# Optimization experiments

Hardware: AMD Instinct MI355X
Metric: run time of the kernel (lower is better)

The kernel has to match this reference:

```python
import jax, jax.numpy as jnp
import numpy as np
import math

B, S, HID = 2, 2048, 2048
NH, NKV, HD, RD = 16, 4, 128, 64  # heads, kv heads, head_dim, rotary dim
G = NH // NKV                      # GQA group size = 4
EPS = 1e-6
THETA = 10000.0


def setup_inputs() -> dict:
    key = jax.random.key(0)
    k0, k1, k2 = jax.random.split(key, 3)
    hidden_states = jax.random.normal(k0, (B, S, HID), dtype=jnp.float32)
    # real rotary embeddings for rope_dim=64
    inv_freq = 1.0 / (THETA ** (jnp.arange(0, RD, 2, dtype=jnp.float32) / RD))  # [32]
    freqs = jnp.arange(S, dtype=jnp.float32)[:, None] * inv_freq[None, :]       # [S,32]
    emb = jnp.concatenate([freqs, freqs], axis=-1)                              # [S,64]
    cos = jnp.broadcast_to(jnp.cos(emb)[None], (B, S, RD)).astype(jnp.float32)
    sin = jnp.broadcast_to(jnp.sin(emb)[None], (B, S, RD)).astype(jnp.float32)
    w_qkv = jax.random.normal(k1, ((NH + 2 * NKV) * HD, HID), dtype=jnp.float32) * 0.02
    q_ln_w = jnp.ones((HD,), dtype=jnp.float32)
    k_ln_w = jnp.ones((HD,), dtype=jnp.float32)
    w_dense = jax.random.normal(k2, (HID, NH * HD), dtype=jnp.float32) * 0.02
    return {"hidden_states": hidden_states, "cos": cos, "sin": sin,
            "w_qkv": w_qkv, "q_ln_w": q_ln_w, "k_ln_w": k_ln_w, "w_dense": w_dense}


def _rmsnorm(x, w):
    xf = x.astype(jnp.float32)
    var = jnp.mean(xf * xf, axis=-1, keepdims=True)
    return (w * (xf * jax.lax.rsqrt(var + EPS)).astype(x.dtype))


def _rotate_half(x):
    x1, x2 = x[..., : x.shape[-1] // 2], x[..., x.shape[-1] // 2:]
    return jnp.concatenate([-x2, x1], axis=-1)


def reference(hidden_states, cos, sin, w_qkv, q_ln_w, k_ln_w, w_dense):
    bsz, q_len, _ = hidden_states.shape
    # fused QKV projection
    qkv = jnp.einsum('bsh,oh->bso', hidden_states, w_qkv)
    qkv = qkv.reshape(bsz, q_len, NH + 2 * NKV, HD)
    q = qkv[:, :, :NH].transpose(0, 2, 1, 3)            # [B,NH,S,HD]
    k = qkv[:, :, NH:NH + NKV].transpose(0, 2, 1, 3)    # [B,NKV,S,HD]
    v = qkv[:, :, NH + NKV:].transpose(0, 2, 1, 3)      # [B,NKV,S,HD]
    # per-head RMSNorm on Q/K
    q = _rmsnorm(q, q_ln_w)
    k = _rmsnorm(k, k_ln_w)
    # partial RoPE on first RD dims
    c = cos[:, None, :, :]  # [B,1,S,RD]
    s = sin[:, None, :, :]
    q_rot = q[..., :RD] * c + _rotate_half(q[..., :RD]) * s
    k_rot = k[..., :RD] * c + _rotate_half(k[..., :RD]) * s
    q = jnp.concatenate([q_rot, q[..., RD:]], axis=-1)
    k = jnp.concatenate([k_rot, k[..., RD:]], axis=-1)
    # GQA: group Q heads over KV heads (equivalent to repeat_kv)
    qg = q.reshape(bsz, NKV, G, q_len, HD)
    scale = 1.0 / math.sqrt(HD)
    scores = jnp.einsum('bgrqd,bgkd->bgrqk', qg, k) * scale   # [B,NKV,G,S,S]
    probs = jax.nn.softmax(scores.astype(jnp.float32), axis=-1).astype(q.dtype)
    out = jnp.einsum('bgrqk,bgkd->bgrqd', probs, v)           # [B,NKV,G,S,HD]
    out = out.reshape(bsz, NH, q_len, HD).transpose(0, 2, 1, 3).reshape(bsz, q_len, NH * HD)
    return jnp.einsum('bsd,od->bso', out, w_dense)
```

## Files before the change

### kernel.cpp

```cpp
#include <hip/hip_runtime.h>
#include <cstdint>
#include <cstddef>

typedef unsigned short u16;
typedef __attribute__((ext_vector_type(8))) short bf16x8;
typedef __attribute__((ext_vector_type(8))) u16   u16x8;
typedef __attribute__((ext_vector_type(4))) short short4v;
typedef __attribute__((ext_vector_type(4))) float f32x4;
typedef __attribute__((ext_vector_type(16))) float f32x16;
typedef __attribute__((ext_vector_type(4))) unsigned int u32x4;

#define DEVI static __device__ __forceinline__

constexpr int B_   = 2;
constexpr int S_   = 2048;
constexpr int HID_ = 2048;
constexpr int NH_  = 16;
constexpr int NKV_ = 4;
constexpr int HD_  = 128;
constexpr int TOK  = B_ * S_;
constexpr int OQKV = (NH_ + 2*NKV_) * HD_;

DEVI u16 f2bf(float f) {
  uint32_t u = __builtin_bit_cast(uint32_t, f);
  return (u16)((u + 0x7fffu + ((u >> 16) & 1u)) >> 16);
}
DEVI float bf2f(u16 h) { return __builtin_bit_cast(float, (uint32_t)h << 16); }

DEVI void gll16(const void* g, void* l) {
  __builtin_amdgcn_global_load_lds(
      (const __attribute__((address_space(1))) uint32_t*)g,
      (__attribute__((address_space(3))) uint32_t*)l, 16, 0, 0);
}

__global__ __launch_bounds__(256) void cvt3_kernel(
    const float* __restrict__ i0, u16* __restrict__ o0, int n0,
    const float* __restrict__ i1, u16* __restrict__ o1, int n1,
    const float* __restrict__ i2, u16* __restrict__ o2, int n2) {
  int idx = blockIdx.x * 256 + threadIdx.x;
  int stride = gridDim.x * 256;
#pragma unroll 1
  for (int pass = 0; pass < 3; ++pass) {
    const float* in = pass == 0 ? i0 : pass == 1 ? i1 : i2;
    u16* out       = pass == 0 ? o0 : pass == 1 ? o1 : o2;
    int n8         = pass == 0 ? n0 : pass == 1 ? n1 : n2;
    for (int i = idx; i < n8; i += stride) {
      const float4* p = reinterpret_cast<const float4*>(in) + (size_t)i * 2;
      float4 a = p[0], b = p[1];
      u16x8 v;
      v[0] = f2bf(a.x); v[1] = f2bf(a.y); v[2] = f2bf(a.z); v[3] = f2bf(a.w);
      v[4] = f2bf(b.x); v[5] = f2bf(b.y); v[6] = f2bf(b.z); v[7] = f2bf(b.w);
      reinterpret_cast<u16x8*>(out)[i] = v;
    }
  }
}

template <bool OUT_BF16>
__global__ __launch_bounds__(256) void gemm_bt_kernel(
    const u16* __restrict__ A, const u16* __restrict__ B, void* __restrict__ Cv,
    int M, int N, int K) {
  constexpr int BM = 128, BN = 128, BK = 32;
  __shared__ __align__(16) u16 As[2][BM * BK];
  __shared__ __align__(16) u16 Bs[2][BN * BK];
  const int tid  = threadIdx.x;
  const int lane = tid & 63;
  const int wid  = tid >> 6;
  const int bm = blockIdx.x * BM;
  const int bn = blockIdx.y * BN;
  const int wm = (wid >> 1) * 64;
  const int wn = (wid & 1) * 64;
  const int fr = lane & 15, fg = lane >> 4;

  const f32x4 fzero = {0.f, 0.f, 0.f, 0.f};
  f32x4 acc[4][4];
#pragma unroll
  for (int m = 0; m < 4; m++)
#pragma unroll
    for (int n = 0; n < 4; n++) acc[m][n] = fzero;

  auto stage = [&](int buf, int k0) {
#pragma unroll
    for (int i = 0; i < 2; i++) {
      int e = i * 256 + tid;
      gll16(A + (size_t)(bm + (e >> 2)) * K + (k0 + (e & 3) * 8), &As[buf][e * 8]);
    }
#pragma unroll
    for (int i = 0; i < 2; i++) {
      int e = i * 256 + tid;
      gll16(B + (size_t)(bn + (e >> 2)) * K + (k0 + (e & 3) * 8), &Bs[buf][e * 8]);
    }
  };

  stage(0, 0);
  __syncthreads();
  const int nt = K / BK;
  for (int t = 0; t < nt; ++t) {
    int cur = t & 1;
    if (t + 1 < nt) stage(cur ^ 1, (t + 1) * BK);
    bf16x8 af[4], bfv[4];
#pragma unroll
    for (int m = 0; m < 4; m++)
      af[m] = *reinterpret_cast<const bf16x8*>(&As[cur][(wm + m * 16 + fr) * BK + fg * 8]);
#pragma unroll
    for (int n = 0; n < 4; n++)
      bfv[n] = *reinterpret_cast<const bf16x8*>(&Bs[cur][(wn + n * 16 + fr) * BK + fg * 8]);
#pragma unroll
    for (int m = 0; m < 4; m++)
#pragma unroll
      for (int n = 0; n < 4; n++)
        acc[m][n] = __builtin_amdgcn_mfma_f32_16x16x32_bf16(af[m], bfv[n], acc[m][n], 0, 0, 0);
    __syncthreads();
  }

#pragma unroll
  for (int m = 0; m < 4; m++)
#pragma unroll
    for (int n = 0; n < 4; n++)
#pragma unroll
      for (int j = 0; j < 4; j++) {
        size_t row = bm + wm + m * 16 + fg * 4 + j;
        size_t col = bn + wn + n * 16 + fr;
        if constexpr (OUT_BF16)
          reinterpret_cast<u16*>(Cv)[row * N + col] = f2bf(acc[m][n][j]);
        else
          reinterpret_cast<float*>(Cv)[row * N + col] = acc[m][n][j];
      }
}

__global__ __launch_bounds__(256) void rmsrope_kernel(
    const u16* __restrict__ qkv, const float* __restrict__ cosb,
    const float* __restrict__ sinb, const float* __restrict__ qw,
    const float* __restrict__ kw, u16* __restrict__ Q, u16* __restrict__ K) {
  int gw   = blockIdx.x * 4 + (threadIdx.x >> 6);
  int lane = threadIdx.x & 63;
  int tok  = gw / 20;
  int slot = gw - tok * 20;
  if (tok >= TOK) return;
  int b = tok >> 11, s = tok & (S_ - 1);
  const u16* src = qkv + (size_t)tok * OQKV + slot * HD_;
  float x0 = bf2f(src[lane]);
  float x1 = bf2f(src[lane + 64]);
  float ss = x0 * x0 + x1 * x1;
#pragma unroll
  for (int m = 1; m < 64; m <<= 1) ss += __shfl_xor(ss, m, 64);
  float r = rsqrtf(ss * (1.0f / 128.0f) + 1e-6f);
  const float* w = (slot < 16) ? qw : kw;
  x0 *= r * w[lane];
  x1 *= r * w[lane + 64];
  float c  = cosb[(size_t)tok * 64 + lane];
  float sn = sinb[(size_t)tok * 64 + lane];
  float partner = __shfl_xor(x0, 32, 64);
  float rot = (lane < 32) ? -partner : partner;
  x0 = x0 * c + rot * sn;
  const float QSC = 0.12751743f;
  u16* dst;
  if (slot < 16) {
    x0 *= QSC; x1 *= QSC;
    dst = Q + (((size_t)b * NH_ + slot) * S_ + s) * HD_;
  } else {
    dst = K + (((size_t)b * NKV_ + (slot - 16)) * S_ + s) * HD_;
  }
  dst[lane]      = f2bf(x0);
  dst[lane + 64] = f2bf(x1);
}

__global__ __launch_bounds__(512, 2) void attn_kernel(
    const u16* __restrict__ Q, const u16* __restrict__ K,
    const u16* __restrict__ QKVb, u16* __restrict__ O) {
  __shared__ __align__(16) u16 Ks[2][64 * 128];
  __shared__ __align__(16) u16 Vt[2][128 * 64];
  __shared__ float rs_lds[8][32];
  const int tid  = threadIdx.x;
  const int lane = tid & 63, wid = tid >> 6;
  const int q32 = lane & 31, hi = lane >> 5;
  const int i_   = blockIdx.x;
  const int xcd  = i_ & 7, s_ = i_ >> 3;
  const int b = xcd >> 2, kvh = xcd & 3;
  const int h = kvh * 4 + (s_ & 3);
  const int qt = s_ >> 2;

  const u16* Qrow  = Q + ((size_t)(b * NH_ + h) * S_ + qt * 256 + wid * 32 + q32) * HD_;
  const u16* Kbase = K + (size_t)(b * NKV_ + kvh) * S_ * HD_;
  const u16* Vbase = QKVb + (size_t)b * S_ * OQKV + (size_t)(NH_ + NKV_) * HD_ + (size_t)kvh * HD_;

  bf16x8 qf[8];
#pragma unroll
  for (int m = 0; m < 8; m++)
    qf[m] = *reinterpret_cast<const bf16x8*>(Qrow + m * 16 + hi * 8);

  f32x16 acc[4];
#pragma unroll
  for (int n = 0; n < 4; n++)
#pragma unroll
    for (int r = 0; r < 16; r++) acc[n][r] = 0.f;

  float rs = 0.f;

  auto stageK = [&](int buf, int kt) {
#pragma unroll
    for (int i = 0; i < 2; i++) {
      int e = i * 512 + tid;
      int krow = e >> 4, ci = e & 15;
      int cs = ci ^ (krow & 15);
      gll16(Kbase + ((size_t)kt * 64 + krow) * HD_ + cs * 8, &Ks[buf][e * 8]);
    }
  };
  u16x8 vreg[4];
  auto loadV = [&](int kt) {
    if (tid < 256) {
      int kvb = tid >> 4, db = tid & 15;
#pragma unroll
      for (int i = 0; i < 4; i++)
        vreg[i] = *reinterpret_cast<const u16x8*>(
            Vbase + ((size_t)kt * 64 + kvb * 4 + i) * OQKV + db * 8);
    }
  };
  auto writeV = [&](int buf) {
    if (tid < 256) {
      int kvb = tid >> 4, db = tid & 15;
#pragma unroll
      for (int j = 0; j < 8; j++) {
        int d = db * 8 + j;
        int sw = (d ^ (d >> 3)) & 7;
        int off = d * 128 + ((((kvb >> 1) ^ sw)) << 4) + ((kvb & 1) << 3);
        short4v wv = {(short)vreg[0][j], (short)vreg[1][j],
                      (short)vreg[2][j], (short)vreg[3][j]};
        *reinterpret_cast<short4v*>(reinterpret_cast<char*>(Vt[buf]) + off) = wv;
      }
    }
  };

  stageK(0, 0);
  loadV(0);
  writeV(0);
  __syncthreads();

  const int NT = S_ / 64;
  for (int kt = 0; kt < NT; ++kt) {
    const int cur = kt & 1;
    if (kt + 1 < NT) { stageK(cur ^ 1, kt + 1); loadV(kt + 1); }

    const u16* kbp = &Ks[cur][(size_t)q32 * 128];
    const int swz = lane & 15;
    unsigned int pa[4][4];
#pragma unroll
    for (int kb = 0; kb < 2; kb++) {
      f32x16 s;
#pragma unroll
      for (int r = 0; r < 16; r++) s[r] = 0.f;
      __builtin_amdgcn_s_setprio(1);
#pragma unroll
      for (int m = 0; m < 8; m++) {
        bf16x8 kf = *reinterpret_cast<const bf16x8*>(
            kbp + kb * 32 * 128 + ((((m * 2 + hi) ^ swz)) << 3));
        s = __builtin_amdgcn_mfma_f32_32x32x16_bf16(kf, qf[m], s, 0, 0, 0);
      }
      __builtin_amdgcn_s_setprio(0);
      float p[16];
#pragma unroll
      for (int r = 0; r < 16; r++) {
        p[r] = exp2f(s[r]);
        rs += p[r];
      }
      unsigned int w[8];
#pragma unroll
      for (int m2 = 0; m2 < 8; m2++) {
        unsigned int wv;
        asm("v_cvt_pk_bf16_f32 %0, %1, %2" : "=v"(wv) : "v"(p[2 * m2]), "v"(p[2 * m2 + 1]));
        w[m2] = wv;
      }
#pragma unroll
      for (int tp = 0; tp < 2; tp++) {
        unsigned int a0 = w[4 * tp + 0], b0 = w[4 * tp + 2];
        unsigned int a1 = w[4 * tp + 1], b1 = w[4 * tp + 3];
        asm("v_permlane32_swap_b32 %0, %1" : "+v"(a0), "+v"(b0));
        asm("v_permlane32_swap_b32 %0, %1" : "+v"(a1), "+v"(b1));
        pa[kb * 2 + tp][0] = a0;
        pa[kb * 2 + tp][1] = a1;
        pa[kb * 2 + tp][2] = b0;
        pa[kb * 2 + tp][3] = b1;
      }
    }

#pragma unroll
    for (int t = 0; t < 4; t++) {
      union { u32x4 u; bf16x8 h; } pf;
      pf.u = (u32x4){pa[t][0], pa[t][1], pa[t][2], pa[t][3]};
      __builtin_amdgcn_s_setprio(1);
#pragma unroll
      for (int n = 0; n < 4; n++) {
        int d = n * 32 + q32;
        int sw = (d ^ (d >> 3)) & 7;
        bf16x8 vf = *reinterpret_cast<const bf16x8*>(
            reinterpret_cast<const char*>(Vt[cur]) + d * 128 + (((t * 2 + hi) ^ sw) << 4));
        acc[n] = __builtin_amdgcn_mfma_f32_32x32x16_bf16(pf.h, vf, acc[n], 0, 0, 0);
      }
      __builtin_amdgcn_s_setprio(0);
    }

    if (kt + 1 < NT) writeV(cur ^ 1);
    __syncthreads();
  }

  float rtot = rs + __shfl_xor(rs, 32, 64);
  if (lane < 32) rs_lds[wid][q32] = rtot;
  __syncthreads();
  float rinv[16];
#pragma unroll
  for (int r = 0; r < 16; r++)
    rinv[r] = 1.0f / rs_lds[wid][(r & 3) + 8 * (r >> 2) + 4 * hi];

  const int qrow0 = qt * 256 + wid * 32;
  u16* ob = O + ((size_t)b * S_ + qrow0) * HID_ + h * HD_ + q32;
#pragma unroll
  for (int n = 0; n < 4; n++)
#pragma unroll
    for (int r = 0; r < 16; r++) {
      int qr = (r & 3) + 8 * (r >> 2) + 4 * hi;
      ob[(size_t)qr * HID_ + n * 32] = f2bf(acc[n][r] * rinv[r]);
    }
}

extern "C" void kernel_launch(void* const* d_in, const int* in_sizes, int n_in,
                              void* d_out, int out_size, void* d_ws, size_t ws_size,
                              hipStream_t stream) {
  (void)in_sizes; (void)n_in; (void)out_size; (void)ws_size;
  const float* hs   = (const float*)d_in[0];
  const float* cosb = (const float*)d_in[1];
  const float* sinb = (const float*)d_in[2];
  const float* wqkv = (const float*)d_in[3];
  const float* qw   = (const float*)d_in[4];
  const float* kw   = (const float*)d_in[5];
  const float* wd   = (const float*)d_in[6];
  float* out = (float*)d_out;
  char* ws = (char*)d_ws;
  constexpr size_t MB = 1048576;
  u16* Xb    = (u16*)(ws + 0 * MB);
  u16* Wqkvb = (u16*)(ws + 16 * MB);
  u16* Wdb   = (u16*)(ws + 28 * MB);
  u16* QKVb  = (u16*)(ws + 36 * MB);
  u16* Qb    = (u16*)(ws + 60 * MB);
  u16* Kb    = (u16*)(ws + 76 * MB);
  u16* Ob    = (u16*)(ws + 80 * MB);

  cvt3_kernel<<<2048, 256, 0, stream>>>(hs, Xb, TOK * HID_ / 8,
                                        wqkv, Wqkvb, OQKV * HID_ / 8,
                                        wd, Wdb, HID_ * HID_ / 8);

  gemm_bt_kernel<true><<<dim3(TOK / 128, OQKV / 128), 256, 0, stream>>>(
      Xb, Wqkvb, QKVb, TOK, OQKV, HID_);

  rmsrope_kernel<<<TOK * 20 / 4, 256, 0, stream>>>(QKVb, cosb, sinb, qw, kw, Qb, Kb);

  attn_kernel<<<256, 512, 0, stream>>>(Qb, Kb, QKVb, Ob);

  gemm_bt_kernel<false><<<dim3(TOK / 128, HID_ / 128), 256, 0, stream>>>(
      Ob, Wdb, out, TOK, HID_, HID_);
}
```

Before: 224.0 us.

## Rewrite GEMM with 256x128x64 tiles, triple-buffered LDS, swizzle and 32x32 MFMA

```diff
diff --git a/kernel.cpp b/kernel.cpp
--- a/kernel.cpp
+++ b/kernel.cpp
@@ -56,74 +56,96 @@
 }
 
 template <bool OUT_BF16>
-__global__ __launch_bounds__(256) void gemm_bt_kernel(
+__global__ __launch_bounds__(512, 1) void gemm_bt2_kernel(
     const u16* __restrict__ A, const u16* __restrict__ B, void* __restrict__ Cv,
     int M, int N, int K) {
-  constexpr int BM = 128, BN = 128, BK = 32;
-  __shared__ __align__(16) u16 As[2][BM * BK];
-  __shared__ __align__(16) u16 Bs[2][BN * BK];
+  constexpr int BM = 256, BN = 128, BK = 64;
+  __shared__ __align__(16) u16 As[3][BM * BK];
+  __shared__ __align__(16) u16 Bs[3][BN * BK];
   const int tid  = threadIdx.x;
-  const int lane = tid & 63;
-  const int wid  = tid >> 6;
+  const int lane = tid & 63, wid = tid >> 6;
+  const int hi   = lane >> 5;
   const int bm = blockIdx.x * BM;
   const int bn = blockIdx.y * BN;
   const int wm = (wid >> 1) * 64;
   const int wn = (wid & 1) * 64;
-  const int fr = lane & 15, fg = lane >> 4;
-
-  const f32x4 fzero = {0.f, 0.f, 0.f, 0.f};
-  f32x4 acc[4][4];
-#pragma unroll
-  for (int m = 0; m < 4; m++)
-#pragma unroll
-    for (int n = 0; n < 4; n++) acc[m][n] = fzero;
-
-  auto stage = [&](int buf, int k0) {
+
+  f32x16 acc[2][2];
+#pragma unroll
+  for (int mf = 0; mf < 2; mf++)
+#pragma unroll
+    for (int nf = 0; nf < 2; nf++)
+#pragma unroll
+      for (int r = 0; r < 16; r++) acc[mf][nf][r] = 0.f;
+
+  auto stage = [&](int t) {
+    int buf = t % 3;
+    const int k0 = t * BK;
+#pragma unroll
+    for (int i = 0; i < 4; i++) {
+      int e = i * 512 + tid;
+      int row = e >> 3, c = e & 7;
+      int cs = c ^ (row & 7);
+      gll16(A + (size_t)(bm + row) * K + (k0 + cs * 8), &As[buf][e * 8]);
+    }
 #pragma unroll
     for (int i = 0; i < 2; i++) {
-      int e = i * 256 + tid;
-      gll16(A + (size_t)(bm + (e >> 2)) * K + (k0 + (e & 3) * 8), &As[buf][e * 8]);
-    }
-#pragma unroll
-    for (int i = 0; i < 2; i++) {
-      int e = i * 256 + tid;
-      gll16(B + (size_t)(bn + (e >> 2)) * K + (k0 + (e & 3) * 8), &Bs[buf][e * 8]);
+      int e = i * 512 + tid;
+      int row = e >> 3, c = e & 7;
+      int cs = c ^ (row & 7);
+      gll16(B + (size_t)(bn + row) * K + (k0 + cs * 8), &Bs[buf][e * 8]);
     }
   };
 
-  stage(0, 0);
-  __syncthreads();
   const int nt = K / BK;
+  stage(0);
+  stage(1);
+  asm volatile("s_waitcnt vmcnt(6)" ::: "memory");
+  __builtin_amdgcn_s_barrier();
+
+  const int r7 = lane & 7;
   for (int t = 0; t < nt; ++t) {
-    int cur = t & 1;
-    if (t + 1 < nt) stage(cur ^ 1, (t + 1) * BK);
-    bf16x8 af[4], bfv[4];
-#pragma unroll
-    for (int m = 0; m < 4; m++)
-      af[m] = *reinterpret_cast<const bf16x8*>(&As[cur][(wm + m * 16 + fr) * BK + fg * 8]);
-#pragma unroll
-    for (int n = 0; n < 4; n++)
-      bfv[n] = *reinterpret_cast<const bf16x8*>(&Bs[cur][(wn + n * 16 + fr) * BK + fg * 8]);
-#pragma unroll
-    for (int m = 0; m < 4; m++)
-#pragma unroll
-      for (int n = 0; n < 4; n++)
-        acc[m][n] = __builtin_amdgcn_mfma_f32_16x16x32_bf16(af[m], bfv[n], acc[m][n], 0, 0, 0);
-    __syncthreads();
+    const int cur = t % 3;
+    if (t + 2 < nt) stage(t + 2);
+    const u16* ab = &As[cur][(size_t)(wm + (lane & 31)) * BK];
+    const u16* bb = &Bs[cur][(size_t)(wn + (lane & 31)) * BK];
+#pragma unroll
+    for (int k16 = 0; k16 < 4; k16++) {
+      const int kc = k16 * 2 + hi;
+      bf16x8 af[2], bfr[2];
+#pragma unroll
+      for (int mf = 0; mf < 2; mf++)
+        af[mf] = *reinterpret_cast<const bf16x8*>(ab + mf * 32 * BK + ((kc ^ r7) << 3));
+#pragma unroll
+      for (int nf = 0; nf < 2; nf++)
+        bfr[nf] = *reinterpret_cast<const bf16x8*>(bb + nf * 32 * BK + ((kc ^ r7) << 3));
+      __builtin_amdgcn_s_setprio(1);
+#pragma unroll
+      for (int mf = 0; mf < 2; mf++)
+#pragma unroll
+        for (int nf = 0; nf < 2; nf++)
+          acc[mf][nf] = __builtin_amdgcn_mfma_f32_32x32x16_bf16(af[mf], bfr[nf], acc[mf][nf], 0, 0, 0);
+      __builtin_amdgcn_s_setprio(0);
+    }
+    if (t + 2 < nt)
+      asm volatile("s_waitcnt vmcnt(6)" ::: "memory");
+    else if (t + 1 < nt)
+      asm volatile("s_waitcnt vmcnt(0)" ::: "memory");
+    __builtin_amdgcn_s_barrier();
   }
 
 #pragma unroll
-  for (int m = 0; m < 4; m++)
-#pragma unroll
-    for (int n = 0; n < 4; n++)
-#pragma unroll
-      for (int j = 0; j < 4; j++) {
-        size_t row = bm + wm + m * 16 + fg * 4 + j;
-        size_t col = bn + wn + n * 16 + fr;
+  for (int mf = 0; mf < 2; mf++)
+#pragma unroll
+    for (int nf = 0; nf < 2; nf++)
+#pragma unroll
+      for (int r = 0; r < 16; r++) {
+        size_t row = bm + wm + mf * 32 + (r & 3) + 8 * (r >> 2) + 4 * hi;
+        size_t col = bn + wn + nf * 32 + (lane & 31);
         if constexpr (OUT_BF16)
-          reinterpret_cast<u16*>(Cv)[row * N + col] = f2bf(acc[m][n][j]);
+          reinterpret_cast<u16*>(Cv)[row * N + col] = f2bf(acc[mf][nf][r]);
         else
-          reinterpret_cast<float*>(Cv)[row * N + col] = acc[m][n][j];
+          reinterpret_cast<float*>(Cv)[row * N + col] = acc[mf][nf][r];
       }
 }
 
@@ -347,13 +369,13 @@
                                         wqkv, Wqkvb, OQKV * HID_ / 8,
                                         wd, Wdb, HID_ * HID_ / 8);
 
-  gemm_bt_kernel<true><<<dim3(TOK / 128, OQKV / 128), 256, 0, stream>>>(
+  gemm_bt2_kernel<true><<<dim3(TOK / 256, OQKV / 128), 512, 0, stream>>>(
       Xb, Wqkvb, QKVb, TOK, OQKV, HID_);
 
   rmsrope_kernel<<<TOK * 20 / 4, 256, 0, stream>>>(QKVb, cosb, sinb, qw, kw, Qb, Kb);
 
   attn_kernel<<<256, 512, 0, stream>>>(Qb, Kb, QKVb, Ob);
 
-  gemm_bt_kernel<false><<<dim3(TOK / 128, HID_ / 128), 256, 0, stream>>>(
+  gemm_bt2_kernel<false><<<dim3(TOK / 256, HID_ / 128), 512, 0, stream>>>(
       Ob, Wdb, out, TOK, HID_, HID_);
 }
```

Measured after the change: 254.9 us. 1.14x slower.

## Fuse per-head RMSNorm and RoPE into the QKV GEMM epilogue

Applied to the files above, without the earlier changes.

```diff
diff --git a/kernel.cpp b/kernel.cpp
--- a/kernel.cpp
+++ b/kernel.cpp
@@ -127,41 +127,138 @@
       }
 }
 
-__global__ __launch_bounds__(256) void rmsrope_kernel(
-    const u16* __restrict__ qkv, const float* __restrict__ cosb,
-    const float* __restrict__ sinb, const float* __restrict__ qw,
-    const float* __restrict__ kw, u16* __restrict__ Q, u16* __restrict__ K) {
-  int gw   = blockIdx.x * 4 + (threadIdx.x >> 6);
-  int lane = threadIdx.x & 63;
-  int tok  = gw / 20;
-  int slot = gw - tok * 20;
-  if (tok >= TOK) return;
-  int b = tok >> 11, s = tok & (S_ - 1);
-  const u16* src = qkv + (size_t)tok * OQKV + slot * HD_;
-  float x0 = bf2f(src[lane]);
-  float x1 = bf2f(src[lane + 64]);
-  float ss = x0 * x0 + x1 * x1;
-#pragma unroll
-  for (int m = 1; m < 64; m <<= 1) ss += __shfl_xor(ss, m, 64);
-  float r = rsqrtf(ss * (1.0f / 128.0f) + 1e-6f);
-  const float* w = (slot < 16) ? qw : kw;
-  x0 *= r * w[lane];
-  x1 *= r * w[lane + 64];
-  float c  = cosb[(size_t)tok * 64 + lane];
-  float sn = sinb[(size_t)tok * 64 + lane];
-  float partner = __shfl_xor(x0, 32, 64);
-  float rot = (lane < 32) ? -partner : partner;
-  x0 = x0 * c + rot * sn;
-  const float QSC = 0.12751743f;
-  u16* dst;
-  if (slot < 16) {
-    x0 *= QSC; x1 *= QSC;
-    dst = Q + (((size_t)b * NH_ + slot) * S_ + s) * HD_;
-  } else {
-    dst = K + (((size_t)b * NKV_ + (slot - 16)) * S_ + s) * HD_;
-  }
-  dst[lane]      = f2bf(x0);
-  dst[lane + 64] = f2bf(x1);
+__global__ __launch_bounds__(256) void gemm_qkv_kernel(
+    const u16* __restrict__ A, const u16* __restrict__ B,
+    u16* __restrict__ QKVb, u16* __restrict__ Qo, u16* __restrict__ Ko,
+    const float* __restrict__ cosb, const float* __restrict__ sinb,
+    const float* __restrict__ qw, const float* __restrict__ kw) {
+  constexpr int N = OQKV, K = HID_;
+  constexpr int BM = 128, BN = 128, BK = 32;
+  __shared__ __align__(16) u16 As[2][BM * BK];
+  __shared__ __align__(16) u16 Bs[2][BN * BK];
+  __shared__ float rsum[4][64];
+  const int tid  = threadIdx.x;
+  const int lane = tid & 63;
+  const int wid  = tid >> 6;
+  const int bm = blockIdx.x * BM;
+  const int bn = blockIdx.y * BN;
+  const int wm = (wid >> 1) * 64;
+  const int wn = (wid & 1) * 64;
+  const int fr = lane & 15, fg = lane >> 4;
+
+  const f32x4 fzero = {0.f, 0.f, 0.f, 0.f};
+  f32x4 acc[4][4];
+#pragma unroll
+  for (int m = 0; m < 4; m++)
+#pragma unroll
+    for (int n = 0; n < 4; n++) acc[m][n] = fzero;
+
+  auto stage = [&](int buf, int k0) {
+#pragma unroll
+    for (int i = 0; i < 2; i++) {
+      int e = i * 256 + tid;
+      gll16(A + (size_t)(bm + (e >> 2)) * K + (k0 + (e & 3) * 8), &As[buf][e * 8]);
+    }
+#pragma unroll
+    for (int i = 0; i < 2; i++) {
+      int e = i * 256 + tid;
+      gll16(B + (size_t)(bn + (e >> 2)) * K + (k0 + (e & 3) * 8), &Bs[buf][e * 8]);
+    }
+  };
+
+  stage(0, 0);
+  __syncthreads();
+  const int nt = K / BK;
+  for (int t = 0; t < nt; ++t) {
+    int cur = t & 1;
+    if (t + 1 < nt) stage(cur ^ 1, (t + 1) * BK);
+    bf16x8 af[4], bfv[4];
+#pragma unroll
+    for (int m = 0; m < 4; m++)
+      af[m] = *reinterpret_cast<const bf16x8*>(&As[cur][(wm + m * 16 + fr) * BK + fg * 8]);
+#pragma unroll
+    for (int n = 0; n < 4; n++)
+      bfv[n] = *reinterpret_cast<const bf16x8*>(&Bs[cur][(wn + n * 16 + fr) * BK + fg * 8]);
+#pragma unroll
+    for (int m = 0; m < 4; m++)
+#pragma unroll
+      for (int n = 0; n < 4; n++)
+        acc[m][n] = __builtin_amdgcn_mfma_f32_16x16x32_bf16(af[m], bfv[n], acc[m][n], 0, 0, 0);
+    __syncthreads();
+  }
+
+  const int slot = blockIdx.y;
+  if (slot >= 20) {
+#pragma unroll
+    for (int m = 0; m < 4; m++)
+#pragma unroll
+      for (int n = 0; n < 4; n++)
+#pragma unroll
+        for (int j = 0; j < 4; j++) {
+          size_t row = bm + wm + m * 16 + fg * 4 + j;
+          size_t col = bn + wn + n * 16 + fr;
+          QKVb[row * N + col] = f2bf(acc[m][n][j]);
+        }
+    return;
+  }
+
+  float ssq[16];
+#pragma unroll
+  for (int m = 0; m < 4; m++)
+#pragma unroll
+    for (int j = 0; j < 4; j++) {
+      float s2 = 0.f;
+#pragma unroll
+      for (int n = 0; n < 4; n++) { float v = acc[m][n][j]; s2 = fmaf(v, v, s2); }
+      ssq[m * 4 + j] = s2;
+    }
+#pragma unroll
+  for (int msk = 1; msk < 16; msk <<= 1)
+#pragma unroll
+    for (int i = 0; i < 16; i++) ssq[i] += __shfl_xor(ssq[i], msk, 64);
+  if (fr == 0) {
+#pragma unroll
+    for (int i = 0; i < 16; i++)
+      rsum[wid][(i >> 2) * 16 + fg * 4 + (i & 3)] = ssq[i];
+  }
+  __syncthreads();
+
+  const float* gam = (slot < 16) ? qw : kw;
+  const float g0 = gam[wn + fr],      g1 = gam[wn + 16 + fr];
+  const float g2 = gam[wn + 32 + fr], g3 = gam[wn + 48 + fr];
+  const float qsc = (slot < 16) ? 0.12751743f : 1.0f;
+
+#pragma unroll
+  for (int m = 0; m < 4; m++)
+#pragma unroll
+    for (int j = 0; j < 4; j++) {
+      const int i = m * 4 + j;
+      float tot = ssq[i] + rsum[wid ^ 1][m * 16 + fg * 4 + j];
+      float rv  = rsqrtf(tot * (1.0f / 128.0f) + 1e-6f);
+      size_t tok = (size_t)(bm + wm + m * 16 + fg * 4 + j);
+      float v0 = acc[m][0][j] * rv * g0, v1 = acc[m][1][j] * rv * g1;
+      float v2 = acc[m][2][j] * rv * g2, v3 = acc[m][3][j] * rv * g3;
+      if (wn == 0) {
+        const float* cb = cosb + tok * 64;
+        const float* sb = sinb + tok * 64;
+        float c0 = cb[fr], c1 = cb[16 + fr], c2 = cb[32 + fr], c3 = cb[48 + fr];
+        float n0 = sb[fr], n1 = sb[16 + fr], n2 = sb[32 + fr], n3 = sb[48 + fr];
+        float t0 = v0 * c0 - v2 * n0;
+        float t1 = v1 * c1 - v3 * n1;
+        float t2 = v2 * c2 + v0 * n2;
+        float t3 = v3 * c3 + v1 * n3;
+        v0 = t0; v1 = t1; v2 = t2; v3 = t3;
+      }
+      v0 *= qsc; v1 *= qsc; v2 *= qsc; v3 *= qsc;
+      int b = (int)(tok >> 11), s = (int)(tok & (S_ - 1));
+      u16* dst = (slot < 16)
+          ? Qo + (((size_t)b * NH_ + slot) * S_ + s) * HD_
+          : Ko + (((size_t)b * NKV_ + (slot - 16)) * S_ + s) * HD_;
+      dst[wn + fr]      = f2bf(v0);
+      dst[wn + 16 + fr] = f2bf(v1);
+      dst[wn + 32 + fr] = f2bf(v2);
+      dst[wn + 48 + fr] = f2bf(v3);
+    }
 }
 
 __global__ __launch_bounds__(512, 2) void attn_kernel(
@@ -347,10 +444,8 @@
                                         wqkv, Wqkvb, OQKV * HID_ / 8,
                                         wd, Wdb, HID_ * HID_ / 8);
 
-  gemm_bt_kernel<true><<<dim3(TOK / 128, OQKV / 128), 256, 0, stream>>>(
-      Xb, Wqkvb, QKVb, TOK, OQKV, HID_);
-
-  rmsrope_kernel<<<TOK * 20 / 4, 256, 0, stream>>>(QKVb, cosb, sinb, qw, kw, Qb, Kb);
+  gemm_qkv_kernel<<<dim3(TOK / 128, OQKV / 128), 256, 0, stream>>>(
+      Xb, Wqkvb, QKVb, Qb, Kb, cosb, sinb, qw, kw);
 
   attn_kernel<<<256, 512, 0, stream>>>(Qb, Kb, QKVb, Ob);
 
```

After: 252.5 us. 1.13x slower.
